# Kernel optimization log

Measured on AMD Instinct MI355X. Metric: run time of the kernel, lower is better.

Reference implementation:

```python
import jax, jax.numpy as jnp
import numpy as np

SEQ_LEN, BATCH, EMB, HID, VOCAB = 8192, 40, 64, 40, 201


def _lstm_cell(x, h, c, Wih, Whh, b):
    # torch gate order: i, f, g, o
    gates = x @ Wih.T + h @ Whh.T + b  # (B, 4H)
    i, f, g, o = jnp.split(gates, 4, axis=-1)
    c_new = jax.nn.sigmoid(f) * c + jax.nn.sigmoid(i) * jnp.tanh(g)
    h_new = jax.nn.sigmoid(o) * jnp.tanh(c_new)
    return h_new, c_new


def setup_inputs() -> dict:
    key = jax.random.key(0)
    ks = jax.random.split(key, 11)
    k = 1.0 / np.sqrt(HID)
    u = lambda kk, shp: jax.random.uniform(kk, shp, jnp.float32, -k, k)
    return {
        "source": jax.random.randint(ks[0], (SEQ_LEN, BATCH), 0, VOCAB),
        "decoder_input": jax.random.normal(ks[1], (1, BATCH, HID), jnp.float32),
        "emb": jax.random.normal(ks[2], (VOCAB, EMB), jnp.float32),
        "enc_Wih": u(ks[3], (4 * HID, EMB)),
        "enc_Whh": u(ks[4], (4 * HID, HID)),
        "enc_bih": u(ks[5], (4 * HID,)),
        "enc_bhh": u(ks[6], (4 * HID,)),
        "dec_Wih": u(ks[7], (4 * HID, HID)),
        "dec_Whh": u(ks[8], (4 * HID, HID)),
        "dec_bih": u(ks[9], (4 * HID,)),
        "dec_bhh": u(ks[10], (4 * HID,)),
    }


def reference(source, decoder_input, emb, enc_Wih, enc_Whh, enc_bih, enc_bhh,
              dec_Wih, dec_Whh, dec_bih, dec_bhh):
    B = source.shape[1]  # == 40, forced by torch.randn(1,40,40)
    embedded = emb[source]  # (S, B, E)
    enc_b = enc_bih + enc_bhh
    dec_b = dec_bih + dec_bhh

    def enc_step(carry, x_t):
        h, c = carry
        h, c = _lstm_cell(x_t, h, c, enc_Wih, enc_Whh, enc_b)
        return (h, c), None

    h0 = jnp.zeros((B, HID), embedded.dtype)
    (h, c), _ = jax.lax.scan(enc_step, (h0, h0), embedded)

    def dec_step(carry, _):
        x, h, c = carry
        h, c = _lstm_cell(x, h, c, dec_Wih, dec_Whh, dec_b)
        return (h, h, c), h  # next input is the output h

    x0 = decoder_input[0]  # (B, H)
    T = B  # loop runs source.size(1) times in the original
    _, outs = jax.lax.scan(dec_step, (x0, h, c), None, length=T)  # (T, B, H)
    # original stacks (1,B,H) slices on dim=1 -> (1, T, B, H)
    return outs[None]
```

## Files before the change

kernel.cpp:

```cpp
#include <hip/hip_runtime.h>
#include <stdint.h>

#define SEQ 8192
#define B   40
#define EMBD 64
#define HID 40
#define VOCAB 201
#define LOG2E 1.4426950408889634f

typedef _Float16 v2h __attribute__((ext_vector_type(2)));
typedef float    v4f __attribute__((ext_vector_type(4)));

__device__ __forceinline__ float fexp2(float x) { float r; asm("v_exp_f32 %0, %1" : "=v"(r) : "v"(x)); return r; }
__device__ __forceinline__ float frcp (float x) { float r; asm("v_rcp_f32 %0, %1" : "=v"(r) : "v"(x)); return r; }
__device__ __forceinline__ float sigm (float x) { return frcp(1.f + fexp2(-LOG2E * x)); }
__device__ __forceinline__ float tanh_(float x) { return fmaf(2.f, frcp(1.f + fexp2(-2.f * LOG2E * x)), -1.f); }
__device__ __forceinline__ v2h rdpair(v2h v, int k) {
    int r = __builtin_amdgcn_readlane(__builtin_bit_cast(int, v), k);
    return __builtin_bit_cast(v2h, r);
}
__device__ __forceinline__ v2h pkrtz(float lo, float hi) {
    return __builtin_bit_cast(v2h, __builtin_amdgcn_cvt_pkrtz(lo, hi));
}
template <int CTRL>
__device__ __forceinline__ float dppq(float v) {
    return __builtin_bit_cast(float,
        __builtin_amdgcn_update_dpp(0, __builtin_bit_cast(int, v), CTRL, 0xF, 0xF, true));
}

__global__ void setup_kernel(const float* __restrict__ emb, const float* __restrict__ Wih,
                             const float* __restrict__ bih, const float* __restrict__ bhh,
                             float4* __restrict__ table4) {
    const int v = blockIdx.x;
    const int e = threadIdx.x;
    if (e >= HID) return;
    const float* er = emb + v * EMBD;
    float acc[4];
#pragma unroll
    for (int g = 0; g < 4; ++g) {
        const int j = g * HID + e;
        const float* wr = Wih + j * EMBD;
        float a = bih[j] + bhh[j];
#pragma unroll 8
        for (int k = 0; k < EMBD; ++k) a = fmaf(er[k], wr[k], a);
        acc[g] = a;
    }
    table4[v * HID + e] = make_float4(acc[0], acc[1], acc[2], acc[3]);
}

__global__ __attribute__((amdgpu_flat_work_group_size(64, 64), amdgpu_waves_per_eu(1, 1)))
void enc_kernel(const int* __restrict__ src,
                const float* __restrict__ Whh,
                const float4* __restrict__ tbl,
                float* __restrict__ est) {
    const int b    = blockIdx.x;
    const int lane = threadIdx.x;
    const int e    = (lane < HID) ? lane : 0;

    __shared__ int ssrc[SEQ];
    for (int t = lane; t < SEQ; t += 64) ssrc[t] = src[t * B + b];

    v2h wi[20], wf[20], wg[20], wo[20];
#pragma unroll
    for (int r = 0; r < 10; ++r) {
        float4 ai = *reinterpret_cast<const float4*>(&Whh[(0 * HID + e) * HID + 4 * r]);
        float4 af = *reinterpret_cast<const float4*>(&Whh[(1 * HID + e) * HID + 4 * r]);
        float4 ag = *reinterpret_cast<const float4*>(&Whh[(2 * HID + e) * HID + 4 * r]);
        float4 ao = *reinterpret_cast<const float4*>(&Whh[(3 * HID + e) * HID + 4 * r]);
        wi[2*r]   = (v2h){(_Float16)ai.x, (_Float16)ai.y};
        wi[2*r+1] = (v2h){(_Float16)ai.z, (_Float16)ai.w};
        wf[2*r]   = (v2h){(_Float16)af.x, (_Float16)af.y};
        wf[2*r+1] = (v2h){(_Float16)af.z, (_Float16)af.w};
        wg[2*r]   = (v2h){(_Float16)ag.x, (_Float16)ag.y};
        wg[2*r+1] = (v2h){(_Float16)ag.z, (_Float16)ag.w};
        wo[2*r]   = (v2h){(_Float16)ao.x, (_Float16)ao.y};
        wo[2*r+1] = (v2h){(_Float16)ao.z, (_Float16)ao.w};
    }

    __syncthreads();

    asm volatile("s_waitcnt vmcnt(0)" ::: "memory");

    const uint64_t base = (uint64_t)(const void*)tbl;
    v4f tq[4];
    int idxw[4];
#pragma unroll
    for (int p = 0; p < 4; ++p) {
        uint64_t a = base + ((uint64_t)(uint32_t)(ssrc[p] * HID + e) << 4);
        asm volatile("global_load_dwordx4 %0, %1, off" : "=v"(tq[p]) : "v"(a));
        idxw[p] = ssrc[p + 4];
    }

    float c = 0.f, h = 0.f;
    v2h hpk = (v2h){(_Float16)0.f, (_Float16)0.f};

#pragma unroll 4
    for (int t = 0; t < SEQ; ++t) {
        const int s = t & 3;

        asm volatile("s_waitcnt vmcnt(3)");
        __builtin_amdgcn_sched_barrier(0);
        v4f q = tq[s];

        float AI = q.x, AF = q.y, AG = q.z, AO = q.w;
#pragma unroll
        for (int m = 0; m < 20; ++m) {
            v2h hm = rdpair(hpk, 2 * m);
            AI = __builtin_amdgcn_fdot2(wi[m], hm, AI, false);
            AF = __builtin_amdgcn_fdot2(wf[m], hm, AF, false);
            AG = __builtin_amdgcn_fdot2(wg[m], hm, AG, false);
            AO = __builtin_amdgcn_fdot2(wo[m], hm, AO, false);
        }
        float si = sigm(AI), sf = sigm(AF), tg = tanh_(AG), so = sigm(AO);
        c = fmaf(sf, c, si * tg);
        h = so * tanh_(c);

        float hA = dppq<0xA0>(h);
        float hB = dppq<0xF5>(h);
        hpk = pkrtz(hA, hB);

        uint64_t a = base + ((uint64_t)(uint32_t)(idxw[s] * HID + e) << 4);
        asm volatile("global_load_dwordx4 %0, %1, off" : "=v"(tq[s]) : "v"(a));
        idxw[s] = ssrc[(t + 8) & (SEQ - 1)];
    }

    if (lane < HID) {
        est[b * 80 + lane]       = h;
        est[b * 80 + HID + lane] = c;
    }
}

__global__ __launch_bounds__(192, 1) void dec_kernel(const float* __restrict__ dinp,
                                                     const float* __restrict__ Wih,
                                                     const float* __restrict__ Whh,
                                                     const float* __restrict__ bih,
                                                     const float* __restrict__ bhh,
                                                     const float* __restrict__ est,
                                                     float* __restrict__ out) {
    const int b    = blockIdx.x;
    const int tid  = threadIdx.x;
    const int lane = tid & 63;
    const int w    = tid >> 6;
    const int tt   = lane >> 4;
    const int q    = lane & 15;
    const int e    = 16 * w + q;
    const bool valid = (e < HID);
    const bool own   = valid && (tt == 0);
    const int j    = tt * HID + (valid ? e : 0);

    __shared__ __align__(16) float hbuf[2][48];

    float4 wi4[10], wh4[10];
#pragma unroll
    for (int r = 0; r < 10; ++r) {
        float4 ti = *reinterpret_cast<const float4*>(&Wih[j * HID + 4 * r]);
        float4 th = *reinterpret_cast<const float4*>(&Whh[j * HID + 4 * r]);
        if (!valid) { ti = make_float4(0,0,0,0); th = make_float4(0,0,0,0); }
        wi4[r] = ti; wh4[r] = th;
    }
    const float bj = valid ? (bih[j] + bhh[j]) : 0.f;

    const float mcoef = (tt == 2) ? (-2.f * LOG2E) : (-LOG2E);
    const float vsc   = (tt == 2) ? 2.f : 1.f;
    const float voff  = (tt == 2) ? -1.f : 0.f;

    float4 xr4[10], hr4[10];
#pragma unroll
    for (int r = 0; r < 10; ++r) {
        xr4[r] = *reinterpret_cast<const float4*>(&dinp[b * HID + 4 * r]);
        hr4[r] = *reinterpret_cast<const float4*>(&est[b * 80 + 4 * r]);
    }
    float c = valid ? est[b * 80 + HID + e] : 0.f;

    for (int t = 0; t < B; ++t) {
        float a0 = bj, a1 = 0.f, a2 = 0.f, a3 = 0.f;
#pragma unroll
        for (int r = 0; r < 10; ++r) {
            a0 = fmaf(wi4[r].x, xr4[r].x, a0);
            a1 = fmaf(wi4[r].y, xr4[r].y, a1);
            a2 = fmaf(wi4[r].z, xr4[r].z, a2);
            a3 = fmaf(wi4[r].w, xr4[r].w, a3);
            a0 = fmaf(wh4[r].x, hr4[r].x, a0);
            a1 = fmaf(wh4[r].y, hr4[r].y, a1);
            a2 = fmaf(wh4[r].z, hr4[r].z, a2);
            a3 = fmaf(wh4[r].w, hr4[r].w, a3);
        }
        float xg = (a0 + a1) + (a2 + a3);

        float E   = fexp2(mcoef * xg);
        float v   = frcp(1.f + E);
        float act = fmaf(vsc, v, voff);

        float ig = __shfl(act, q);
        float fg = __shfl(act, q + 16);
        float gg = __shfl(act, q + 32);
        float og = __shfl(act, q + 48);

        c = fmaf(fg, c, ig * gg);
        float Ec = fexp2(-2.f * LOG2E * c);
        float th = fmaf(2.f, frcp(1.f + Ec), -1.f);
        float h  = og * th;

        if (own) out[(t * B + b) * HID + e] = h;

        if (own) hbuf[t & 1][e] = h;
        __syncthreads();
#pragma unroll
        for (int r = 0; r < 10; ++r) {
            hr4[r] = *reinterpret_cast<const float4*>(&hbuf[t & 1][4 * r]);
            xr4[r] = hr4[r];
        }
    }
}

extern "C" void kernel_launch(void* const* d_in, const int* in_sizes, int n_in,
                              void* d_out, int out_size, void* d_ws, size_t ws_size,
                              hipStream_t stream) {
    const int*   src  = (const int*)  d_in[0];
    const float* dinp = (const float*)d_in[1];
    const float* emb  = (const float*)d_in[2];
    const float* eWih = (const float*)d_in[3];
    const float* eWhh = (const float*)d_in[4];
    const float* ebih = (const float*)d_in[5];
    const float* ebhh = (const float*)d_in[6];
    const float* dWih = (const float*)d_in[7];
    const float* dWhh = (const float*)d_in[8];
    const float* dbih = (const float*)d_in[9];
    const float* dbhh = (const float*)d_in[10];
    float* out = (float*)d_out;

    float4* table4 = (float4*)d_ws;
    float*  est    = (float*)(table4 + VOCAB * HID);

    hipLaunchKernelGGL(setup_kernel, dim3(VOCAB), dim3(64), 0, stream, emb, eWih, ebih, ebhh, table4);
    hipLaunchKernelGGL(enc_kernel,   dim3(B),     dim3(64), 0, stream, src, eWhh, table4, est);
    hipLaunchKernelGGL(dec_kernel,   dim3(B),     dim3(192), 0, stream, dinp, dWih, dWhh, dbih, dbhh, est, out);
}
```

Baseline: 2.262 ms.

## Split encoder LSTM gates across four waves with LDS exchange per step

The encoder block grows from one wave to four, and each wave computes one gate (i, f, g, o) with its own 20 fp16 weight pairs. This replaces the four sequential dot-product chains per lane with one. The gate table is laid out gate-major so each wave loads a single dword per step. Gate activations are exchanged through double-buffered shared memory with a __syncthreads every timestep. That barrier sits on the serial recurrence path and may cost more than the dot-product work it removes.

```diff
diff --git a/kernel.cpp b/kernel.cpp
--- a/kernel.cpp
+++ b/kernel.cpp
@@ -9,11 +9,9 @@
 #define LOG2E 1.4426950408889634f
 
 typedef _Float16 v2h __attribute__((ext_vector_type(2)));
-typedef float    v4f __attribute__((ext_vector_type(4)));
 
 __device__ __forceinline__ float fexp2(float x) { float r; asm("v_exp_f32 %0, %1" : "=v"(r) : "v"(x)); return r; }
 __device__ __forceinline__ float frcp (float x) { float r; asm("v_rcp_f32 %0, %1" : "=v"(r) : "v"(x)); return r; }
-__device__ __forceinline__ float sigm (float x) { return frcp(1.f + fexp2(-LOG2E * x)); }
 __device__ __forceinline__ float tanh_(float x) { return fmaf(2.f, frcp(1.f + fexp2(-2.f * LOG2E * x)), -1.f); }
 __device__ __forceinline__ v2h rdpair(v2h v, int k) {
     int r = __builtin_amdgcn_readlane(__builtin_bit_cast(int, v), k);
@@ -30,12 +28,11 @@
 
 __global__ void setup_kernel(const float* __restrict__ emb, const float* __restrict__ Wih,
                              const float* __restrict__ bih, const float* __restrict__ bhh,
-                             float4* __restrict__ table4) {
+                             float* __restrict__ tabg) {
     const int v = blockIdx.x;
     const int e = threadIdx.x;
     if (e >= HID) return;
     const float* er = emb + v * EMBD;
-    float acc[4];
 #pragma unroll
     for (int g = 0; g < 4; ++g) {
         const int j = g * HID + e;
@@ -43,51 +40,52 @@
         float a = bih[j] + bhh[j];
 #pragma unroll 8
         for (int k = 0; k < EMBD; ++k) a = fmaf(er[k], wr[k], a);
-        acc[g] = a;
-    }
-    table4[v * HID + e] = make_float4(acc[0], acc[1], acc[2], acc[3]);
-}
-
-__global__ __attribute__((amdgpu_flat_work_group_size(64, 64), amdgpu_waves_per_eu(1, 1)))
+        tabg[(g * VOCAB + v) * HID + e] = a;
+    }
+}
+
+__global__ __attribute__((amdgpu_flat_work_group_size(256, 256), amdgpu_waves_per_eu(1, 1)))
 void enc_kernel(const int* __restrict__ src,
                 const float* __restrict__ Whh,
-                const float4* __restrict__ tbl,
+                const float* __restrict__ tabg,
                 float* __restrict__ est) {
     const int b    = blockIdx.x;
-    const int lane = threadIdx.x;
+    const int tid  = threadIdx.x;
+    const int lane = tid & 63;
+    const int wg   = tid >> 6;
     const int e    = (lane < HID) ? lane : 0;
 
     __shared__ int ssrc[SEQ];
-    for (int t = lane; t < SEQ; t += 64) ssrc[t] = src[t * B + b];
-
-    v2h wi[20], wf[20], wg[20], wo[20];
-#pragma unroll
-    for (int r = 0; r < 10; ++r) {
-        float4 ai = *reinterpret_cast<const float4*>(&Whh[(0 * HID + e) * HID + 4 * r]);
-        float4 af = *reinterpret_cast<const float4*>(&Whh[(1 * HID + e) * HID + 4 * r]);
-        float4 ag = *reinterpret_cast<const float4*>(&Whh[(2 * HID + e) * HID + 4 * r]);
-        float4 ao = *reinterpret_cast<const float4*>(&Whh[(3 * HID + e) * HID + 4 * r]);
-        wi[2*r]   = (v2h){(_Float16)ai.x, (_Float16)ai.y};
-        wi[2*r+1] = (v2h){(_Float16)ai.z, (_Float16)ai.w};
-        wf[2*r]   = (v2h){(_Float16)af.x, (_Float16)af.y};
-        wf[2*r+1] = (v2h){(_Float16)af.z, (_Float16)af.w};
-        wg[2*r]   = (v2h){(_Float16)ag.x, (_Float16)ag.y};
-        wg[2*r+1] = (v2h){(_Float16)ag.z, (_Float16)ag.w};
-        wo[2*r]   = (v2h){(_Float16)ao.x, (_Float16)ao.y};
-        wo[2*r+1] = (v2h){(_Float16)ao.z, (_Float16)ao.w};
-    }
+    __shared__ __align__(16) float act[2][48][4];
+
+    for (int t = tid; t < SEQ; t += 256) ssrc[t] = src[t * B + b];
+
+    v2h w[20];
+    {
+        const float* row = &Whh[(wg * HID + e) * HID];
+#pragma unroll
+        for (int r = 0; r < 10; ++r) {
+            float4 a4 = *reinterpret_cast<const float4*>(&row[4 * r]);
+            w[2*r]   = (v2h){(_Float16)a4.x, (_Float16)a4.y};
+            w[2*r+1] = (v2h){(_Float16)a4.z, (_Float16)a4.w};
+        }
+    }
+    const float mcoef = (wg == 2) ? (-2.f * LOG2E) : (-LOG2E);
+    const float vsc   = (wg == 2) ? 2.f : 1.f;
+    const float voff  = (wg == 2) ? -1.f : 0.f;
 
     __syncthreads();
 
     asm volatile("s_waitcnt vmcnt(0)" ::: "memory");
 
-    const uint64_t base = (uint64_t)(const void*)tbl;
-    v4f tq[4];
+    const uint64_t base = (uint64_t)(const void*)tabg
+                        + ((uint64_t)(uint32_t)(wg * VOCAB * HID + e) << 2);
+    float tq[4];
     int idxw[4];
 #pragma unroll
     for (int p = 0; p < 4; ++p) {
-        uint64_t a = base + ((uint64_t)(uint32_t)(ssrc[p] * HID + e) << 4);
-        asm volatile("global_load_dwordx4 %0, %1, off" : "=v"(tq[p]) : "v"(a));
+        uint64_t a = base + (uint64_t)((uint32_t)(ssrc[p] * HID) << 2);
+        asm volatile("global_load_dword %0, %1, off" : "=v"(tq[p]) : "v"(a));
         idxw[p] = ssrc[p + 4];
     }
 
@@ -97,36 +95,38 @@
 #pragma unroll 4
     for (int t = 0; t < SEQ; ++t) {
         const int s = t & 3;
+        const int p = t & 1;
 
         asm volatile("s_waitcnt vmcnt(3)");
         __builtin_amdgcn_sched_barrier(0);
-        v4f q = tq[s];
-
-        float AI = q.x, AF = q.y, AG = q.z, AO = q.w;
+        float A = tq[s];
+
 #pragma unroll
         for (int m = 0; m < 20; ++m) {
             v2h hm = rdpair(hpk, 2 * m);
-            AI = __builtin_amdgcn_fdot2(wi[m], hm, AI, false);
-            AF = __builtin_amdgcn_fdot2(wf[m], hm, AF, false);
-            AG = __builtin_amdgcn_fdot2(wg[m], hm, AG, false);
-            AO = __builtin_amdgcn_fdot2(wo[m], hm, AO, false);
-        }
-        float si = sigm(AI), sf = sigm(AF), tg = tanh_(AG), so = sigm(AO);
-        c = fmaf(sf, c, si * tg);
-        h = so * tanh_(c);
+            A = __builtin_amdgcn_fdot2(w[m], hm, A, false);
+        }
+        float a_ = fmaf(vsc, frcp(1.f + fexp2(mcoef * A)), voff);
+
+        act[p][e][wg] = a_;
+        __syncthreads();
+        float4 g4 = *reinterpret_cast<const float4*>(&act[p][e][0]);
+
+        c = fmaf(g4.y, c, g4.x * g4.z);
+        h = g4.w * tanh_(c);
 
         float hA = dppq<0xA0>(h);
         float hB = dppq<0xF5>(h);
         hpk = pkrtz(hA, hB);
 
-        uint64_t a = base + ((uint64_t)(uint32_t)(idxw[s] * HID + e) << 4);
-        asm volatile("global_load_dwordx4 %0, %1, off" : "=v"(tq[s]) : "v"(a));
+        uint64_t a = base + (uint64_t)((uint32_t)(idxw[s] * HID) << 2);
+        asm volatile("global_load_dword %0, %1, off" : "=v"(tq[s]) : "v"(a));
         idxw[s] = ssrc[(t + 8) & (SEQ - 1)];
     }
 
-    if (lane < HID) {
-        est[b * 80 + lane]       = h;
-        est[b * 80 + HID + lane] = c;
+    if (tid < HID) {
+        est[b * 80 + tid]       = h;
+        est[b * 80 + HID + tid] = c;
     }
 }
 
@@ -229,10 +229,10 @@
     const float* dbhh = (const float*)d_in[10];
     float* out = (float*)d_out;
 
-    float4* table4 = (float4*)d_ws;
-    float*  est    = (float*)(table4 + VOCAB * HID);
-
-    hipLaunchKernelGGL(setup_kernel, dim3(VOCAB), dim3(64), 0, stream, emb, eWih, ebih, ebhh, table4);
-    hipLaunchKernelGGL(enc_kernel,   dim3(B),     dim3(64), 0, stream, src, eWhh, table4, est);
+    float* tabg = (float*)d_ws;
+    float* est  = tabg + 4 * VOCAB * HID;
+
+    hipLaunchKernelGGL(setup_kernel, dim3(VOCAB), dim3(64),  0, stream, emb, eWih, ebih, ebhh, tabg);
+    hipLaunchKernelGGL(enc_kernel,   dim3(B),     dim3(256), 0, stream, src, eWhh, tabg, est);
     hipLaunchKernelGGL(dec_kernel,   dim3(B),     dim3(192), 0, stream, dinp, dWih, dWhh, dbih, dbhh, est, out);
 }
```

After: 1.853 ms (median of 2 runs). -18.1%, faster.
